# Performance work log

Hardware: AMD Instinct MI355X
Metric: run time of the kernel (lower is better)

Reference implementation:

```python
import jax, jax.numpy as jnp
import numpy as np

B, S, D, H = 2, 2048, 1024, 16
DEPTH = D // H
NEG = -1e9


def setup_inputs() -> dict:
    key = jax.random.key(0)
    ks = jax.random.split(key, 8)
    scale = 1.0 / np.sqrt(D)
    inp = {
        "query": jax.random.normal(ks[0], (B, S, D), jnp.float32),
        "key": jax.random.normal(ks[1], (B, S, D), jnp.float32),
        "value": jax.random.normal(ks[2], (B, S, D), jnp.float32),
        # causal look-ahead mask: 1 where attention is disallowed
        "mask": (1.0 - jnp.tril(jnp.ones((S, S), jnp.float32)))[None, None, :, :],
        "Wq": jax.random.normal(ks[3], (D, D), jnp.float32) * scale,
        "Wk": jax.random.normal(ks[4], (D, D), jnp.float32) * scale,
        "Wv": jax.random.normal(ks[5], (D, D), jnp.float32) * scale,
        "Wo": jax.random.normal(ks[6], (D, D), jnp.float32) * scale,
        "bq": jnp.zeros((D,), jnp.float32),
        "bk": jnp.zeros((D,), jnp.float32),
        "bv": jnp.zeros((D,), jnp.float32),
        "bo": jnp.zeros((D,), jnp.float32),
    }
    return inp


def _split_heads(x):
    # [B,S,D] -> [B,H,S,depth]
    return x.reshape(B, -1, H, DEPTH).transpose(0, 2, 1, 3)


def reference(query, key, value, mask, Wq, Wk, Wv, Wo, bq, bk, bv, bo):
    q = _split_heads(query @ Wq + bq)
    k = _split_heads(key @ Wk + bk)
    v = _split_heads(value @ Wv + bv)
    logits = jnp.einsum("bhqd,bhkd->bhqk", q, k) / jnp.sqrt(jnp.float32(DEPTH))
    logits = logits + mask * NEG
    attn = jax.nn.softmax(logits, axis=-1)
    ctx = jnp.einsum("bhqk,bhkd->bhqd", attn, v)  # [B,H,S,depth]
    concat = ctx.transpose(0, 2, 1, 3).reshape(B, -1, D)
    return concat @ Wo + bo
```

## Files before the change

kernel.cpp:

```cpp
#include <hip/hip_runtime.h>
#include <hip/hip_bf16.h>
#include <stdint.h>

#define BB 2
#define SS 2048
#define DDIM 1024
#define HH 16
#define DEPTH 64
#define MROWS (BB*SS)

typedef short bf16x8 __attribute__((ext_vector_type(8)));
typedef float f32x4 __attribute__((ext_vector_type(4)));

__device__ inline ushort f2bf(float f) {
  union { float f; unsigned u; } v; v.f = f;
  unsigned r = v.u + 0x7fffu + ((v.u >> 16) & 1u);
  return (ushort)(r >> 16);
}

__device__ inline uint pkbf(float a, float b) {
  uint r;
  asm("v_cvt_pk_bf16_f32 %0, %1, %2" : "=v"(r) : "v"(a), "v"(b));
  return r;
}

__device__ inline void gload_lds16(const void* g, void* l) {
  __builtin_amdgcn_global_load_lds(
      (const __attribute__((address_space(1))) unsigned*)g,
      (__attribute__((address_space(3))) unsigned*)l,
      16, 0, 0);
}

__global__ void wprep_kernel(const float* __restrict__ W0, const float* __restrict__ W1,
                             const float* __restrict__ W2, const float* __restrict__ W3,
                             ushort* __restrict__ T0, ushort* __restrict__ T1,
                             ushort* __restrict__ T2, ushort* __restrict__ T3) {
  __shared__ float tile[32][33];
  int z = blockIdx.x >> 10;
  int rr = blockIdx.x & 1023;
  const float* W = (z == 0) ? W0 : (z == 1) ? W1 : (z == 2) ? W2 : W3;
  ushort* T = (z == 0) ? T0 : (z == 1) ? T1 : (z == 2) ? T2 : T3;
  int tx = threadIdx.x & 31, ty = threadIdx.x >> 5;
  int n0 = (rr & 31) * 32, k0 = (rr >> 5) * 32;
#pragma unroll
  for (int i = 0; i < 4; i++)
    tile[ty + i * 8][tx] = W[(size_t)(k0 + ty + i * 8) * DDIM + n0 + tx];
  __syncthreads();
#pragma unroll
  for (int i = 0; i < 4; i++) {
    int n = n0 + ty + i * 8;
    int col = (z < 3) ? (k0 + (tx ^ ((n & 3) << 3))) : (k0 + tx);
    T[(size_t)n * DDIM + col] = f2bf(tile[tx][ty + i * 8]);
  }
}

__global__ __launch_bounds__(256, 4) void qkv_gemm_kernel(
    const float* __restrict__ Aq, const float* __restrict__ Ak, const float* __restrict__ Av,
    const ushort* __restrict__ Wqt, const ushort* __restrict__ Wkt, const ushort* __restrict__ Wvt,
    const float* __restrict__ bqp, const float* __restrict__ bkp, const float* __restrict__ bvp,
    ushort* __restrict__ Qh, ushort* __restrict__ Kh, ushort* __restrict__ Vtg) {
  const int id = blockIdx.x;
  const int xcd = id & 7;
  const int rest = id >> 3;
  const int xblk = rest & 7;
  const int slot = rest >> 3;
  const int g = xcd * 12 + slot;
  const int yblk = g & 31;
  const int z = g >> 5;

  const float*  Ap = (z == 0) ? Aq  : (z == 1) ? Ak  : Av;
  const ushort* Bt = (z == 0) ? Wqt : (z == 1) ? Wkt : Wvt;
  const float* bias = (z == 0) ? bqp : (z == 1) ? bkp : bvp;

  __shared__ __align__(16) ushort As[2][128 * 32];
  __shared__ __align__(16) ushort Bs[2][128 * 32];
  const int tid = threadIdx.x;
  const int w = tid >> 6, lane = tid & 63;
  const int m0 = yblk * 128, n0 = xblk * 128;
  const int wr = (w >> 1) * 64, wc = (w & 1) * 64;
  const int l4 = lane >> 4, l15 = lane & 15;
  const int swzf = (l15 & 3) << 3;
  const int arow = tid & 127;
  const int acg  = (tid >> 7) * 16;
  const int aswz = (arow & 3) << 3;
  const size_t abase = (size_t)(m0 + arow) * DDIM;
  const int bsr = lane >> 2;
  const int bsc = (lane & 3) * 8;

  f32x4 zero = {0.f, 0.f, 0.f, 0.f};
  f32x4 acc[4][4];
#pragma unroll
  for (int i = 0; i < 4; i++)
#pragma unroll
    for (int j = 0; j < 4; j++) acc[i][j] = zero;

  float4 areg[4];
#pragma unroll
  for (int j = 0; j < 4; ++j)
    areg[j] = *(const float4*)&Ap[abase + acg + j * 4];
#pragma unroll
  for (int it = 0; it < 2; ++it)
    gload_lds16(Bt + (size_t)(n0 + it * 64 + w * 16 + bsr) * DDIM + bsc,
                &Bs[0][(it * 64 + w * 16) * 32]);
  {
    uint4 p0, p1;
    p0.x = pkbf(areg[0].x, areg[0].y); p0.y = pkbf(areg[0].z, areg[0].w);
    p0.z = pkbf(areg[1].x, areg[1].y); p0.w = pkbf(areg[1].z, areg[1].w);
    p1.x = pkbf(areg[2].x, areg[2].y); p1.y = pkbf(areg[2].z, areg[2].w);
    p1.z = pkbf(areg[3].x, areg[3].y); p1.w = pkbf(areg[3].z, areg[3].w);
    *(uint4*)&As[0][arow * 32 + (acg ^ aswz)]       = p0;
    *(uint4*)&As[0][arow * 32 + ((acg + 8) ^ aswz)] = p1;
  }
#pragma unroll
  for (int j = 0; j < 4; ++j)
    areg[j] = *(const float4*)&Ap[abase + 32 + acg + j * 4];
  __syncthreads();

  int b = 0;
  for (int t = 0; t < 32; ++t) {
    if (t < 31) {
#pragma unroll
      for (int it = 0; it < 2; ++it)
        gload_lds16(Bt + (size_t)(n0 + it * 64 + w * 16 + bsr) * DDIM + (t + 1) * 32 + bsc,
                    &Bs[b ^ 1][(it * 64 + w * 16) * 32]);
      uint4 p0, p1;
      p0.x = pkbf(areg[0].x, areg[0].y); p0.y = pkbf(areg[0].z, areg[0].w);
      p0.z = pkbf(areg[1].x, areg[1].y); p0.w = pkbf(areg[1].z, areg[1].w);
      p1.x = pkbf(areg[2].x, areg[2].y); p1.y = pkbf(areg[2].z, areg[2].w);
      p1.z = pkbf(areg[3].x, areg[3].y); p1.w = pkbf(areg[3].z, areg[3].w);
      *(uint4*)&As[b ^ 1][arow * 32 + (acg ^ aswz)]       = p0;
      *(uint4*)&As[b ^ 1][arow * 32 + ((acg + 8) ^ aswz)] = p1;
      if (t < 30) {
#pragma unroll
        for (int j = 0; j < 4; ++j)
          areg[j] = *(const float4*)&Ap[abase + (t + 2) * 32 + acg + j * 4];
      }
    }
    bf16x8 bfr[4];
#pragma unroll
    for (int n = 0; n < 4; ++n)
      bfr[n] = *(const bf16x8*)&Bs[b][(wc + n * 16 + l15) * 32 + ((l4 * 8) ^ swzf)];
#pragma unroll
    for (int m = 0; m < 4; ++m) {
      bf16x8 af = *(const bf16x8*)&As[b][(wr + m * 16 + l15) * 32 + ((l4 * 8) ^ swzf)];
#pragma unroll
      for (int n = 0; n < 4; ++n)
        acc[m][n] = __builtin_amdgcn_mfma_f32_16x16x32_bf16(af, bfr[n], acc[m][n], 0, 0, 0);
    }
    __syncthreads();
    b ^= 1;
  }

  if (z != 2) {
    ushort* outp = (z == 0) ? Qh : Kh;
    ushort* wtile = (w < 2) ? &As[w][0] : &Bs[w - 2][0];
    const int gcol0 = n0 + wc;
    const int hh = gcol0 >> 6;
    const int bb = m0 >> 11;
    const int s0g = (m0 + wr) & (SS - 1);
#pragma unroll
    for (int m = 0; m < 4; m++) {
#pragma unroll
      for (int n = 0; n < 4; n++) {
        int dloc = n * 16 + l15;
        float bv = bias[gcol0 + dloc];
#pragma unroll
        for (int r = 0; r < 4; r++) {
          int sloc = m * 16 + l4 * 4 + r;
          wtile[sloc * 64 + (dloc ^ ((sloc & 7) << 3))] = f2bf(acc[m][n][r] + bv);
        }
      }
    }
#pragma unroll
    for (int i = 0; i < 8; ++i) {
      int srow = i * 8 + (lane >> 3);
      int dch = (lane & 7) * 8;
      bf16x8 val = *(const bf16x8*)&wtile[srow * 64 + (dch ^ ((srow & 7) << 3))];
      *(bf16x8*)&outp[((size_t)(bb * HH + hh) * SS + s0g + srow) * DEPTH + dch] = val;
    }
  } else {
    ushort* wtile = (w < 2) ? &As[w][0] : &Bs[w - 2][0];
    const int gcol0 = n0 + wc;
    const int hh = gcol0 >> 6;
    const int bb = m0 >> 11;
    const int s0g = (m0 + wr) & (SS - 1);
#pragma unroll
    for (int p = 0; p < 2; ++p) {
#pragma unroll
      for (int nn = 0; nn < 2; ++nn) {
        int n = p * 2 + nn;
        int dloc = nn * 16 + l15;
        float bv = bias[gcol0 + p * 32 + dloc];
#pragma unroll
        for (int m = 0; m < 4; m++) {
#pragma unroll
          for (int rr = 0; rr < 4; rr += 2) {
            int sloc = m * 16 + l4 * 4 + rr;
            int gg = (sloc >> 3) ^ (dloc & 7);
            uint pk = pkbf(acc[m][n][rr] + bv, acc[m][n][rr + 1] + bv);
            *(uint*)&wtile[dloc * 64 + gg * 8 + (sloc & 7)] = pk;
          }
        }
      }
      __syncthreads();
#pragma unroll
      for (int i = 0; i < 4; ++i) {
        int dloc = (lane >> 3) + i * 8;
        int gg = (lane & 7) ^ (dloc & 7);
        bf16x8 val = *(const bf16x8*)&wtile[dloc * 64 + gg * 8];
        int dglob = p * 32 + dloc;
        size_t addr = ((size_t)(bb * HH + hh) * DEPTH + dglob) * SS + s0g + (lane & 7) * 8;
        *(bf16x8*)&Vtg[addr] = val;
      }
      __syncthreads();
    }
  }
}

__global__ __launch_bounds__(256, 3) void out_gemm_kernel(
    const ushort* __restrict__ A, const ushort* __restrict__ Bt,
    const float* __restrict__ bias, float* __restrict__ out,
    int M, int N, int K) {
  __shared__ __align__(16) ushort As[2][128 * 64];
  __shared__ __align__(16) ushort Bs[2][64 * 64];
  const int id = blockIdx.x;
  const int xcd = id & 7;
  const int rest = id >> 3;
  const int xblk = rest & 15;
  const int slot = rest >> 4;
  const int yblk = xcd * 4 + slot;

  const int tid = threadIdx.x;
  const int w = tid >> 6, lane = tid & 63;
  const int m0 = yblk * 128, n0 = xblk * 64;
  const int wr = (w >> 1) * 64, wc = (w & 1) * 32;
  const int l4 = lane >> 4, l15 = lane & 15;
  const int srow8 = w * 8 + (lane >> 3);
  const int scol8 = (lane & 7) * 8;

  f32x4 zero = {0.f, 0.f, 0.f, 0.f};
  f32x4 acc[4][2];
#pragma unroll
  for (int i = 0; i < 4; i++)
#pragma unroll
    for (int j = 0; j < 2; j++) acc[i][j] = zero;

#pragma unroll
  for (int it = 0; it < 4; ++it)
    gload_lds16(A + (size_t)(m0 + it * 32 + srow8) * K + scol8,
                &As[0][(it * 32 + w * 8) * 64]);
#pragma unroll
  for (int it = 0; it < 2; ++it)
    gload_lds16(Bt + (size_t)(n0 + it * 32 + srow8) * K + scol8,
                &Bs[0][(it * 32 + w * 8) * 64]);
  __syncthreads();

  int buf = 0;
  for (int t = 0; t < 16; ++t) {
    if (t + 1 < 16) {
#pragma unroll
      for (int it = 0; it < 4; ++it)
        gload_lds16(A + (size_t)(m0 + it * 32 + srow8) * K + (t + 1) * 64 + scol8,
                    &As[buf ^ 1][(it * 32 + w * 8) * 64]);
#pragma unroll
      for (int it = 0; it < 2; ++it)
        gload_lds16(Bt + (size_t)(n0 + it * 32 + srow8) * K + (t + 1) * 64 + scol8,
                    &Bs[buf ^ 1][(it * 32 + w * 8) * 64]);
    }
#pragma unroll
    for (int kk = 0; kk < 2; ++kk) {
      bf16x8 af[4], bfr[2];
#pragma unroll
      for (int m = 0; m < 4; m++)
        af[m] = *(const bf16x8*)&As[buf][(wr + m * 16 + l15) * 64 + kk * 32 + l4 * 8];
#pragma unroll
      for (int n = 0; n < 2; n++)
        bfr[n] = *(const bf16x8*)&Bs[buf][(wc + n * 16 + l15) * 64 + kk * 32 + l4 * 8];
#pragma unroll
      for (int m = 0; m < 4; m++)
#pragma unroll
        for (int n = 0; n < 2; n++)
          acc[m][n] = __builtin_amdgcn_mfma_f32_16x16x32_bf16(af[m], bfr[n], acc[m][n], 0, 0, 0);
    }
    __syncthreads();
    buf ^= 1;
  }

#pragma unroll
  for (int m = 0; m < 4; m++) {
#pragma unroll
    for (int n = 0; n < 2; n++) {
      int col = n0 + wc + n * 16 + l15;
      float bv = bias[col];
#pragma unroll
      for (int r = 0; r < 4; r++) {
        int row = m0 + wr + m * 16 + l4 * 4 + r;
        out[(size_t)row * N + col] = acc[m][n][r] + bv;
      }
    }
  }
}

__global__ __launch_bounds__(256, 4) void attn_kernel(
    const ushort* __restrict__ Qh, const ushort* __restrict__ Kh,
    const ushort* __restrict__ Vt, ushort* __restrict__ ctx) {
  __shared__ __align__(16) ushort Ks[2][64 * 64];
  __shared__ __align__(16) ushort Vs[2][64 * 64];
  __shared__ __align__(16) ushort Ps[4][16 * 64];
  const int tid = threadIdx.x;
  const int w = tid >> 6, lane = tid & 63;
  const int l4 = lane >> 4, l15 = lane & 15;
  const float CE = 0.18033688f;

  const int xcd = blockIdx.x & 7;
  const int local = blockIdx.x >> 3;
  const int bh = xcd * 4 + (local & 3);
  const int chunk = 31 - (local >> 2);
  const int b = bh >> 4, h = bh & 15;
  const size_t qkbase = (size_t)bh * SS * DEPTH;
  const size_t vbase  = (size_t)bh * DEPTH * SS;

  const int srow_w = w * 8 + (lane >> 3);
  const int colb_lin = (lane & 7) * 16;
  const int swz_rd = (l15 & 7) << 3;

  const int q0 = chunk * 64 + w * 16;
  const int nt = chunk + 1;

  bf16x8 aq[2];
#pragma unroll
  for (int cc = 0; cc < 2; cc++)
    aq[cc] = *(const bf16x8*)&Qh[qkbase + (size_t)(q0 + l15) * DEPTH + cc * 32 + l4 * 8];

  f32x4 zero = {0.f, 0.f, 0.f, 0.f};
  f32x4 o[4];
  float m_run = -__builtin_inff(), l_run = 0.f;
#pragma unroll
  for (int d = 0; d < 4; d++) o[d] = zero;

  int buf = 0;
#pragma unroll
  for (int it = 0; it < 2; ++it) {
    int row = it * 32 + srow_w;
    int col_e = (colb_lin ^ ((row & 7) << 4)) >> 1;
    int ldsoff = it * 2048 + w * 512;
    gload_lds16(Kh + qkbase + (size_t)row * DEPTH + col_e, &Ks[0][ldsoff]);
    gload_lds16(Vt + vbase + (size_t)row * SS + col_e, &Vs[0][ldsoff]);
  }
  __syncthreads();

  for (int t = 0; t < nt; ++t) {
    if (t + 1 < nt) {
      const int kv1 = (t + 1) * 64;
#pragma unroll
      for (int it = 0; it < 2; ++it) {
        int row = it * 32 + srow_w;
        int col_e = (colb_lin ^ ((row & 7) << 4)) >> 1;
        int ldsoff = it * 2048 + w * 512;
        gload_lds16(Kh + qkbase + (size_t)(kv1 + row) * DEPTH + col_e, &Ks[buf ^ 1][ldsoff]);
        gload_lds16(Vt + vbase + (size_t)row * SS + kv1 + col_e, &Vs[buf ^ 1][ldsoff]);
      }
    }

    const int kv0 = t * 64;
    f32x4 s[4];
    __builtin_amdgcn_s_setprio(1);
#pragma unroll
    for (int n = 0; n < 4; n++) {
      f32x4 zacc = zero;
      int kr = n * 16 + l15;
#pragma unroll
      for (int cc = 0; cc < 2; cc++) {
        bf16x8 bk = *(const bf16x8*)&Ks[buf][kr * 64 + ((cc * 32 + l4 * 8) ^ swz_rd)];
        zacc = __builtin_amdgcn_mfma_f32_16x16x32_bf16(bk, aq[cc], zacc, 0, 0, 0);
      }
      s[n] = zacc;
    }
    __builtin_amdgcn_s_setprio(0);

    const int qg = q0 + l15;
    if (t == nt - 1) {
#pragma unroll
      for (int n = 0; n < 4; n++) {
        int kb = kv0 + n * 16 + l4 * 4;
#pragma unroll
        for (int r = 0; r < 4; r++)
          if (kb + r > qg) s[n][r] = -1e9f;
      }
    }

    float mx = -__builtin_inff();
#pragma unroll
    for (int n = 0; n < 4; n++)
      mx = fmaxf(mx, fmaxf(fmaxf(s[n][0], s[n][1]), fmaxf(s[n][2], s[n][3])));
    mx = fmaxf(mx, __shfl_xor(mx, 16));
    mx = fmaxf(mx, __shfl_xor(mx, 32));
    if (!__all(mx - m_run <= 44.36f)) {
      float mnew = fmaxf(m_run, mx);
      float alpha = exp2f((m_run - mnew) * CE);
      m_run = mnew;
      l_run *= alpha;
#pragma unroll
      for (int d = 0; d < 4; d++) o[d] *= alpha;
    }
    float mc = m_run * CE;
    float rs = 0.f;
#pragma unroll
    for (int n = 0; n < 4; n++)
#pragma unroll
      for (int r = 0; r < 4; r++) {
        float p = exp2f(s[n][r] * CE - mc);
        s[n][r] = p;
        rs += p;
      }
    l_run += rs;

    ushort* Pw = &Ps[w][0];
#pragma unroll
    for (int n = 0; n < 4; n++) {
      int col = (n * 16 + l4 * 4) ^ swz_rd;
      uint2 pk;
      pk.x = pkbf(s[n][0], s[n][1]);
      pk.y = pkbf(s[n][2], s[n][3]);
      *(uint2*)&Pw[l15 * 64 + col] = pk;
    }

    bf16x8 pa[2];
#pragma unroll
    for (int cc = 0; cc < 2; cc++)
      pa[cc] = *(const bf16x8*)&Pw[l15 * 64 + ((cc * 32 + l4 * 8) ^ swz_rd)];

    __builtin_amdgcn_s_setprio(1);
#pragma unroll
    for (int d = 0; d < 4; d++) {
      int dr = d * 16 + l15;
#pragma unroll
      for (int cc = 0; cc < 2; cc++) {
        bf16x8 av = *(const bf16x8*)&Vs[buf][dr * 64 + ((cc * 32 + l4 * 8) ^ swz_rd)];
        o[d] = __builtin_amdgcn_mfma_f32_16x16x32_bf16(av, pa[cc], o[d], 0, 0, 0);
      }
    }
    __builtin_amdgcn_s_setprio(0);

    __syncthreads();
    buf ^= 1;
  }

  float lv = l_run;
  lv += __shfl_xor(lv, 16);
  lv += __shfl_xor(lv, 32);
  float inv = 1.f / lv;
  size_t rowbase = ((size_t)(b * SS + q0 + l15)) * DDIM + h * DEPTH;
#pragma unroll
  for (int d = 0; d < 4; d++) {
    *(uint*)&ctx[rowbase + d * 16 + l4 * 4]     = pkbf(o[d][0] * inv, o[d][1] * inv);
    *(uint*)&ctx[rowbase + d * 16 + l4 * 4 + 2] = pkbf(o[d][2] * inv, o[d][3] * inv);
  }
}

extern "C" void kernel_launch(void* const* d_in, const int* in_sizes, int n_in,
                              void* d_out, int out_size, void* d_ws, size_t ws_size,
                              hipStream_t stream) {
  const float* query = (const float*)d_in[0];
  const float* key_  = (const float*)d_in[1];
  const float* value = (const float*)d_in[2];
  const float* Wq = (const float*)d_in[4];
  const float* Wk = (const float*)d_in[5];
  const float* Wv = (const float*)d_in[6];
  const float* Wo = (const float*)d_in[7];
  const float* bq = (const float*)d_in[8];
  const float* bk = (const float*)d_in[9];
  const float* bv = (const float*)d_in[10];
  const float* bo = (const float*)d_in[11];

  char* ws = (char*)d_ws;
  const size_t MB = 1u << 20;
  ushort* Wqt = (ushort*)(ws + 24 * MB);
  ushort* Wkt = (ushort*)(ws + 26 * MB);
  ushort* Wvt = (ushort*)(ws + 28 * MB);
  ushort* Wot = (ushort*)(ws + 30 * MB);
  ushort* Qh  = (ushort*)(ws + 32 * MB);
  ushort* Kh  = (ushort*)(ws + 40 * MB);
  ushort* Vtg = (ushort*)(ws + 48 * MB);
  ushort* Cb  = (ushort*)(ws + 56 * MB);

  wprep_kernel<<<4096, 256, 0, stream>>>(Wq, Wk, Wv, Wo, Wqt, Wkt, Wvt, Wot);

  qkv_gemm_kernel<<<768, 256, 0, stream>>>(
      query, key_, value, Wqt, Wkt, Wvt, bq, bk, bv, Qh, Kh, Vtg);

  attn_kernel<<<1024, 256, 0, stream>>>(Qh, Kh, Vtg, Cb);

  out_gemm_kernel<<<512, 256, 0, stream>>>(
      Cb, Wot, bo, (float*)d_out, MROWS, DDIM, DDIM);
}
```

Baseline: 134.3 us.

## Simplify QKV GEMM to single-buffered 128x64 tiles with direct stores

Shrinks the QKV projection tile to 128x64, doubles the grid, and raises the occupancy hint. It drops LDS double buffering, the XOR swizzle (also in weight prep), and the LDS-staged epilogue in favour of direct global stores. The aim is more parallelism and fewer LDS bytes per block. The cost is likely bank conflicts, lost load/compute overlap, uncoalesced output writes and lower operand reuse.

```diff
diff --git a/kernel.cpp b/kernel.cpp
--- a/kernel.cpp
+++ b/kernel.cpp
@@ -47,14 +47,11 @@
     tile[ty + i * 8][tx] = W[(size_t)(k0 + ty + i * 8) * DDIM + n0 + tx];
   __syncthreads();
 #pragma unroll
-  for (int i = 0; i < 4; i++) {
-    int n = n0 + ty + i * 8;
-    int col = (z < 3) ? (k0 + (tx ^ ((n & 3) << 3))) : (k0 + tx);
-    T[(size_t)n * DDIM + col] = f2bf(tile[tx][ty + i * 8]);
-  }
-}
-
-__global__ __launch_bounds__(256, 4) void qkv_gemm_kernel(
+  for (int i = 0; i < 4; i++)
+    T[(size_t)(n0 + ty + i * 8) * DDIM + k0 + tx] = f2bf(tile[tx][ty + i * 8]);
+}
+
+__global__ __launch_bounds__(256, 5) void qkv_gemm_kernel(
     const float* __restrict__ Aq, const float* __restrict__ Ak, const float* __restrict__ Av,
     const ushort* __restrict__ Wqt, const ushort* __restrict__ Wkt, const ushort* __restrict__ Wvt,
     const float* __restrict__ bqp, const float* __restrict__ bkp, const float* __restrict__ bvp,
@@ -62,9 +59,9 @@
   const int id = blockIdx.x;
   const int xcd = id & 7;
   const int rest = id >> 3;
-  const int xblk = rest & 7;
-  const int slot = rest >> 3;
-  const int g = xcd * 12 + slot;
+  const int xblk = rest & 15;
+  const int gslot = rest >> 4;
+  const int g = xcd * 12 + gslot;
   const int yblk = g & 31;
   const int z = g >> 5;
 
@@ -72,147 +69,91 @@
   const ushort* Bt = (z == 0) ? Wqt : (z == 1) ? Wkt : Wvt;
   const float* bias = (z == 0) ? bqp : (z == 1) ? bkp : bvp;
 
-  __shared__ __align__(16) ushort As[2][128 * 32];
-  __shared__ __align__(16) ushort Bs[2][128 * 32];
+  __shared__ __align__(16) ushort As[128 * 32];
+  __shared__ __align__(16) ushort Bs[64 * 32];
   const int tid = threadIdx.x;
   const int w = tid >> 6, lane = tid & 63;
-  const int m0 = yblk * 128, n0 = xblk * 128;
-  const int wr = (w >> 1) * 64, wc = (w & 1) * 64;
+  const int m0 = yblk * 128, n0 = xblk * 64;
+  const int wr = (w >> 1) * 64, wc = (w & 1) * 32;
   const int l4 = lane >> 4, l15 = lane & 15;
-  const int swzf = (l15 & 3) << 3;
   const int arow = tid & 127;
   const int acg  = (tid >> 7) * 16;
-  const int aswz = (arow & 3) << 3;
   const size_t abase = (size_t)(m0 + arow) * DDIM;
-  const int bsr = lane >> 2;
-  const int bsc = (lane & 3) * 8;
+  const int bsrow = w * 16 + (lane >> 2);
+  const int bscol = (lane & 3) * 8;
 
   f32x4 zero = {0.f, 0.f, 0.f, 0.f};
-  f32x4 acc[4][4];
+  f32x4 acc[4][2];
 #pragma unroll
   for (int i = 0; i < 4; i++)
 #pragma unroll
-    for (int j = 0; j < 4; j++) acc[i][j] = zero;
+    for (int j = 0; j < 2; j++) acc[i][j] = zero;
 
   float4 areg[4];
 #pragma unroll
   for (int j = 0; j < 4; ++j)
     areg[j] = *(const float4*)&Ap[abase + acg + j * 4];
-#pragma unroll
-  for (int it = 0; it < 2; ++it)
-    gload_lds16(Bt + (size_t)(n0 + it * 64 + w * 16 + bsr) * DDIM + bsc,
-                &Bs[0][(it * 64 + w * 16) * 32]);
-  {
-    uint4 p0, p1;
-    p0.x = pkbf(areg[0].x, areg[0].y); p0.y = pkbf(areg[0].z, areg[0].w);
-    p0.z = pkbf(areg[1].x, areg[1].y); p0.w = pkbf(areg[1].z, areg[1].w);
-    p1.x = pkbf(areg[2].x, areg[2].y); p1.y = pkbf(areg[2].z, areg[2].w);
-    p1.z = pkbf(areg[3].x, areg[3].y); p1.w = pkbf(areg[3].z, areg[3].w);
-    *(uint4*)&As[0][arow * 32 + (acg ^ aswz)]       = p0;
-    *(uint4*)&As[0][arow * 32 + ((acg + 8) ^ aswz)] = p1;
-  }
-#pragma unroll
-  for (int j = 0; j < 4; ++j)
-    areg[j] = *(const float4*)&Ap[abase + 32 + acg + j * 4];
-  __syncthreads();
-
-  int b = 0;
+
   for (int t = 0; t < 32; ++t) {
-    if (t < 31) {
-#pragma unroll
-      for (int it = 0; it < 2; ++it)
-        gload_lds16(Bt + (size_t)(n0 + it * 64 + w * 16 + bsr) * DDIM + (t + 1) * 32 + bsc,
-                    &Bs[b ^ 1][(it * 64 + w * 16) * 32]);
+    {
       uint4 p0, p1;
       p0.x = pkbf(areg[0].x, areg[0].y); p0.y = pkbf(areg[0].z, areg[0].w);
       p0.z = pkbf(areg[1].x, areg[1].y); p0.w = pkbf(areg[1].z, areg[1].w);
       p1.x = pkbf(areg[2].x, areg[2].y); p1.y = pkbf(areg[2].z, areg[2].w);
       p1.z = pkbf(areg[3].x, areg[3].y); p1.w = pkbf(areg[3].z, areg[3].w);
-      *(uint4*)&As[b ^ 1][arow * 32 + (acg ^ aswz)]       = p0;
-      *(uint4*)&As[b ^ 1][arow * 32 + ((acg + 8) ^ aswz)] = p1;
-      if (t < 30) {
-#pragma unroll
-        for (int j = 0; j < 4; ++j)
-          areg[j] = *(const float4*)&Ap[abase + (t + 2) * 32 + acg + j * 4];
-      }
-    }
-    bf16x8 bfr[4];
-#pragma unroll
-    for (int n = 0; n < 4; ++n)
-      bfr[n] = *(const bf16x8*)&Bs[b][(wc + n * 16 + l15) * 32 + ((l4 * 8) ^ swzf)];
+      *(uint4*)&As[arow * 32 + acg]     = p0;
+      *(uint4*)&As[arow * 32 + acg + 8] = p1;
+    }
+    gload_lds16(Bt + (size_t)(n0 + bsrow) * DDIM + t * 32 + bscol, &Bs[(w * 16) * 32]);
+    if (t < 31) {
+#pragma unroll
+      for (int j = 0; j < 4; ++j)
+        areg[j] = *(const float4*)&Ap[abase + (t + 1) * 32 + acg + j * 4];
+    }
+    __syncthreads();
+    bf16x8 bfr[2];
+#pragma unroll
+    for (int n = 0; n < 2; ++n)
+      bfr[n] = *(const bf16x8*)&Bs[(wc + n * 16 + l15) * 32 + l4 * 8];
 #pragma unroll
     for (int m = 0; m < 4; ++m) {
-      bf16x8 af = *(const bf16x8*)&As[b][(wr + m * 16 + l15) * 32 + ((l4 * 8) ^ swzf)];
-#pragma unroll
-      for (int n = 0; n < 4; ++n)
+      bf16x8 af = *(const bf16x8*)&As[(wr + m * 16 + l15) * 32 + l4 * 8];
+#pragma unroll
+      for (int n = 0; n < 2; ++n)
         acc[m][n] = __builtin_amdgcn_mfma_f32_16x16x32_bf16(af, bfr[n], acc[m][n], 0, 0, 0);
     }
     __syncthreads();
-    b ^= 1;
-  }
-
+  }
+
+  const int hh = n0 >> 6;
+  const int bb = m0 >> 11;
+  const int s0g = (m0 + wr) & (SS - 1);
   if (z != 2) {
     ushort* outp = (z == 0) ? Qh : Kh;
-    ushort* wtile = (w < 2) ? &As[w][0] : &Bs[w - 2][0];
-    const int gcol0 = n0 + wc;
-    const int hh = gcol0 >> 6;
-    const int bb = m0 >> 11;
-    const int s0g = (m0 + wr) & (SS - 1);
 #pragma unroll
     for (int m = 0; m < 4; m++) {
 #pragma unroll
-      for (int n = 0; n < 4; n++) {
-        int dloc = n * 16 + l15;
-        float bv = bias[gcol0 + dloc];
+      for (int n = 0; n < 2; n++) {
+        int dloc = wc + n * 16 + l15;
+        float bv = bias[n0 + dloc];
 #pragma unroll
         for (int r = 0; r < 4; r++) {
-          int sloc = m * 16 + l4 * 4 + r;
-          wtile[sloc * 64 + (dloc ^ ((sloc & 7) << 3))] = f2bf(acc[m][n][r] + bv);
+          int s = s0g + m * 16 + l4 * 4 + r;
+          outp[((size_t)(bb * HH + hh) * SS + s) * DEPTH + dloc] = f2bf(acc[m][n][r] + bv);
         }
       }
     }
-#pragma unroll
-    for (int i = 0; i < 8; ++i) {
-      int srow = i * 8 + (lane >> 3);
-      int dch = (lane & 7) * 8;
-      bf16x8 val = *(const bf16x8*)&wtile[srow * 64 + (dch ^ ((srow & 7) << 3))];
-      *(bf16x8*)&outp[((size_t)(bb * HH + hh) * SS + s0g + srow) * DEPTH + dch] = val;
-    }
   } else {
-    ushort* wtile = (w < 2) ? &As[w][0] : &Bs[w - 2][0];
-    const int gcol0 = n0 + wc;
-    const int hh = gcol0 >> 6;
-    const int bb = m0 >> 11;
-    const int s0g = (m0 + wr) & (SS - 1);
-#pragma unroll
-    for (int p = 0; p < 2; ++p) {
-#pragma unroll
-      for (int nn = 0; nn < 2; ++nn) {
-        int n = p * 2 + nn;
-        int dloc = nn * 16 + l15;
-        float bv = bias[gcol0 + p * 32 + dloc];
-#pragma unroll
-        for (int m = 0; m < 4; m++) {
-#pragma unroll
-          for (int rr = 0; rr < 4; rr += 2) {
-            int sloc = m * 16 + l4 * 4 + rr;
-            int gg = (sloc >> 3) ^ (dloc & 7);
-            uint pk = pkbf(acc[m][n][rr] + bv, acc[m][n][rr + 1] + bv);
-            *(uint*)&wtile[dloc * 64 + gg * 8 + (sloc & 7)] = pk;
-          }
-        }
-      }
-      __syncthreads();
-#pragma unroll
-      for (int i = 0; i < 4; ++i) {
-        int dloc = (lane >> 3) + i * 8;
-        int gg = (lane & 7) ^ (dloc & 7);
-        bf16x8 val = *(const bf16x8*)&wtile[dloc * 64 + gg * 8];
-        int dglob = p * 32 + dloc;
-        size_t addr = ((size_t)(bb * HH + hh) * DEPTH + dglob) * SS + s0g + (lane & 7) * 8;
-        *(bf16x8*)&Vtg[addr] = val;
-      }
-      __syncthreads();
+#pragma unroll
+    for (int m = 0; m < 4; m++) {
+#pragma unroll
+      for (int n = 0; n < 2; n++) {
+        int dloc = wc + n * 16 + l15;
+        float bv = bias[n0 + dloc];
+        size_t rowb = ((size_t)(bb * HH + hh) * DEPTH + dloc) * SS + s0g + m * 16 + l4 * 4;
+        *(uint*)&Vtg[rowb]     = pkbf(acc[m][n][0] + bv, acc[m][n][1] + bv);
+        *(uint*)&Vtg[rowb + 2] = pkbf(acc[m][n][2] + bv, acc[m][n][3] + bv);
+      }
     }
   }
 }
@@ -486,7 +427,7 @@
 
   wprep_kernel<<<4096, 256, 0, stream>>>(Wq, Wk, Wv, Wo, Wqt, Wkt, Wvt, Wot);
 
-  qkv_gemm_kernel<<<768, 256, 0, stream>>>(
+  qkv_gemm_kernel<<<1536, 256, 0, stream>>>(
       query, key_, value, Wqt, Wkt, Wvt, bq, bk, bv, Qh, Kh, Vtg);
 
   attn_kernel<<<1024, 256, 0, stream>>>(Qh, Kh, Vtg, Cb);
```

Result: slower. 178.8 us (+33.1%).
